# Kernel optimization log

Measured on AMD Instinct MI355X. Metric: run time of the kernel, lower is better.

## Reference

```python
import jax, jax.numpy as jnp
import numpy as np

B, L, D, DF, E, R = 4, 1024, 1024, 4096, 32768, 64
EPS = 1e-6


def layer_norm(x, g, b, eps=EPS):
    mu = x.mean(-1, keepdims=True)
    var = ((x - mu) ** 2).mean(-1, keepdims=True)
    return (x - mu) * jax.lax.rsqrt(var + eps) * g + b


def setup_inputs() -> dict:
    key = jax.random.key(0)
    ks = jax.random.split(key, 16)
    s = 0.02
    return {
        "hidden_states": jax.random.normal(ks[0], (B, L, D), jnp.float32),
        "rel_table": jax.random.normal(ks[1], (R, D), jnp.float32) * s,
        "Wq": jax.random.normal(ks[2], (D, D), jnp.float32) * s,
        "bq": jnp.zeros((D,), jnp.float32),
        "Wk": jax.random.normal(ks[3], (D, D), jnp.float32) * s,
        "Wv": jax.random.normal(ks[4], (D, D), jnp.float32) * s,
        "Wo": jax.random.normal(ks[5], (D, D), jnp.float32) * s,
        "bo": jnp.zeros((D,), jnp.float32),
        "ln0_g": jnp.ones((D,), jnp.float32),
        "ln0_b": jnp.zeros((D,), jnp.float32),
        "ln1_g": jnp.ones((D,), jnp.float32),
        "ln1_b": jnp.zeros((D,), jnp.float32),
        "W1": jax.random.normal(ks[6], (D, DF), jnp.float32) * s,
        "b1": jnp.zeros((DF,), jnp.float32),
        "W2": jax.random.normal(ks[7], (DF, D), jnp.float32) * s,
        "b2": jnp.zeros((D,), jnp.float32),
        "ln2_g": jnp.ones((D,), jnp.float32),
        "ln2_b": jnp.zeros((D,), jnp.float32),
        "edge_src": jax.random.randint(ks[8], (B, E), 0, L, jnp.int32),
        "edge_dst": jax.random.randint(ks[9], (B, E), 0, L, jnp.int32),
        "edge_rel": jax.random.randint(ks[10], (B, E), 0, R, jnp.int32),
    }


def reference(hidden_states, rel_table, Wq, bq, Wk, Wv, Wo, bo,
              ln0_g, ln0_b, ln1_g, ln1_b, W1, b1, W2, b2, ln2_g, ln2_b,
              edge_src, edge_dst, edge_rel):
    scale = np.sqrt(D).astype(np.float32)  # num_heads=1 -> d_k = D
    hs_norm = layer_norm(hidden_states, ln0_g, ln0_b)

    def rgat_one(x, src, dst, rel):
        # x: [L, D]; src/dst/rel: [E]
        e = rel_table[rel]                       # [E, D] relation embeddings
        q = x @ Wq + bq
        k = x @ Wk
        v = x @ Wv
        score = jnp.sum((k[src] + e) * q[dst], axis=-1) / scale      # [E]
        score = jnp.exp(jnp.clip(score, -10.0, 10.0))
        wv = jax.ops.segment_sum((v[src] + e) * score[:, None], dst, num_segments=L)
        z = jax.ops.segment_sum(score, dst, num_segments=L)          # [L]
        o = wv / z[:, None]
        out = layer_norm(x + o @ Wo + bo, ln1_g, ln1_b)
        ffn = jnp.maximum(out @ W1 + b1, 0.0) @ W2 + b2
        return layer_norm(out + ffn, ln2_g, ln2_b)

    graph_rep = jax.vmap(rgat_one)(hs_norm, edge_src, edge_dst, edge_rel)
    out = jax.nn.elu(graph_rep)                  # dropout = identity (eval)
    return hidden_states + out
```

## Files before the change

kernel.cpp:

```cpp
#include <hip/hip_runtime.h>
#include <hip/hip_bf16.h>

#define B_SZ 4
#define L_SEQ 1024
#define D_MODEL 1024
#define DF_FF 4096
#define E_PER_B 32768
#define R_REL 64
#define M_ROWS (B_SZ * L_SEQ)

typedef __attribute__((ext_vector_type(8))) short bf16x8;
typedef __attribute__((ext_vector_type(4))) float f32x4;

__device__ inline float b2f(unsigned short u) {
    union { unsigned int i; float f; } x; x.i = ((unsigned int)u) << 16; return x.f;
}
__device__ inline unsigned short f2b(float f) {
    union { float f; unsigned int u; } x; x.f = f;
    unsigned int r = x.u + 0x7FFFu + ((x.u >> 16) & 1u);
    return (unsigned short)(r >> 16);
}

#define GLOBAL_CAST(p) ((const __attribute__((address_space(1))) void*)(p))
#define LDS_CAST(p)    ((__attribute__((address_space(3))) void*)(p))

#define BT_QKV (1024u * 3072u)
#define SEXT_M 1152
#define LDA_WV 1088
#define LDB_WVP 1152
#define BT_WVP (1024u * 1152u)

__global__ void prep_all(const float* __restrict__ Wq, const float* __restrict__ Wk,
                         const float* __restrict__ Wv, const float* __restrict__ Wo,
                         const float* __restrict__ W1, const float* __restrict__ W2,
                         const float* __restrict__ rel, const float* __restrict__ bq,
                         const float* __restrict__ hidden,
                         const float* __restrict__ ln0_g, const float* __restrict__ ln0_b,
                         unsigned short* __restrict__ Wqkv_t, unsigned short* __restrict__ Wo_t,
                         unsigned short* __restrict__ W1_t, unsigned short* __restrict__ W2_t,
                         unsigned short* __restrict__ relbPad,
                         float* __restrict__ bqkv,
                         unsigned short* __restrict__ Xn_b16,
                         float* __restrict__ zeroReg) {
    __shared__ float tile[32][33];
    __shared__ float sb1[4], sb2[4];
    const int id = blockIdx.x, tid = threadIdx.x;
    if (id < 12288) {
        const float* src; unsigned short* dst; int K, N, x, y;
        if (id < 4096) {
            const int seg = id >> 10, t = id & 1023;
            K = 1024; N = 1024; x = t & 31; y = t >> 5;
            src = (seg == 0) ? Wq : (seg == 1) ? Wk : (seg == 2) ? Wv : Wo;
            dst = (seg == 3) ? Wo_t : (Wqkv_t + (size_t)seg * 1048576);
        } else if (id < 8192) {
            const int t = id - 4096; K = 1024; N = 4096; x = t & 127; y = t >> 7;
            src = W1; dst = W1_t;
        } else {
            const int t = id - 8192; K = 4096; N = 1024; x = t & 31; y = t >> 5;
            src = W2; dst = W2_t;
        }
        const int n0 = x * 32, k0 = y * 32, tx = tid & 31, ty = tid >> 5;
#pragma unroll
        for (int r = 0; r < 32; r += 8)
            tile[ty + r][tx] = src[(size_t)(k0 + ty + r) * N + (n0 + tx)];
        __syncthreads();
#pragma unroll
        for (int r = 0; r < 32; r += 8)
            dst[(size_t)(n0 + ty + r) * K + (k0 + tx)] = f2b(tile[tx][ty + r]);
    } else if (id < 12800) {
        const int i = (id - 12288) * 256 + tid;
        relbPad[i] = (i < 65536) ? f2b(rel[i]) : (unsigned short)0;
    } else if (id < 12812) {
        const int i = (id - 12800) * 256 + tid;
        bqkv[i] = (i < 1024) ? bq[i] : 0.0f;
    } else if (id < 16908) {
        const int row = id - 12812, t = tid;
        const size_t base = (size_t)row * 1024 + t * 4;
        float4 xv = *(const float4*)(hidden + base);
        float x0 = xv.x, x1 = xv.y, x2 = xv.z, x3 = xv.w;
        float s = x0 + x1 + x2 + x3;
#pragma unroll
        for (int o = 32; o > 0; o >>= 1) s += __shfl_down(s, o);
        if ((t & 63) == 0) sb1[t >> 6] = s;
        __syncthreads();
        const float mu = (sb1[0] + sb1[1] + sb1[2] + sb1[3]) * (1.0f / 1024.0f);
        const float d0 = x0 - mu, d1 = x1 - mu, d2 = x2 - mu, d3 = x3 - mu;
        float s2 = d0 * d0 + d1 * d1 + d2 * d2 + d3 * d3;
#pragma unroll
        for (int o = 32; o > 0; o >>= 1) s2 += __shfl_down(s2, o);
        if ((t & 63) == 0) sb2[t >> 6] = s2;
        __syncthreads();
        const float var = (sb2[0] + sb2[1] + sb2[2] + sb2[3]) * (1.0f / 1024.0f);
        const float rstd = rsqrtf(var + 1e-6f);
        const float4 gv = *(const float4*)(ln0_g + t * 4);
        const float4 bv = *(const float4*)(ln0_b + t * 4);
        ushort4 ob;
        ob.x = f2b(d0 * rstd * gv.x + bv.x);
        ob.y = f2b(d1 * rstd * gv.y + bv.y);
        ob.z = f2b(d2 * rstd * gv.z + bv.z);
        ob.w = f2b(d3 * rstd * gv.w + bv.w);
        *(ushort4*)(Xn_b16 + base) = ob;
    } else {
        const size_t base = (size_t)(id - 16908) * 4096 + tid * 4;
        const float4 z4 = make_float4(0.f, 0.f, 0.f, 0.f);
#pragma unroll
        for (int j = 0; j < 4; j++)
            *(float4*)(zeroReg + base + j * 1024) = z4;
    }
}

__device__ inline void tile_swizzle(int id, int ntn, int& tm, int& tn) {
    tm = ((id & 7) + ((id >> 3) / ntn) * 8) * 128;
    tn = ((id >> 3) % ntn) * 128;
}
__device__ inline void tsw256(int id, int ntn, int& tm, int& tn) {
    tm = ((id & 7) + ((id >> 3) / ntn) * 8) * 256;
    tn = ((id >> 3) % ntn) * 256;
}

#define GEMM_BODY(GA, LDA_, GB, LDB_, KLEN)                                                 \
    f32x4 acc[4][4];                                                                        \
    _Pragma("unroll") for (int i = 0; i < 4; i++)                                           \
        _Pragma("unroll") for (int j = 0; j < 4; j++) acc[i][j] = (f32x4)0.0f;              \
    for (int k0 = 0; k0 < (KLEN); k0 += 64) {                                               \
        __syncthreads();                                                                    \
        _Pragma("unroll") for (int r = 0; r < 4; ++r) {                                     \
            __builtin_amdgcn_global_load_lds(GLOBAL_CAST((GA) + (size_t)r * 8 * (LDA_)),    \
                LDS_CAST(&lA[(wave * 32 + r * 8) * 64]), 16, 0, 0);                         \
            __builtin_amdgcn_global_load_lds(GLOBAL_CAST((GB) + (size_t)r * 8 * (LDB_)),    \
                LDS_CAST(&lB[(wave * 32 + r * 8) * 64]), 16, 0, 0);                         \
        }                                                                                   \
        (GA) += 64; (GB) += 64;                                                             \
        __builtin_amdgcn_s_waitcnt(0);                                                      \
        __syncthreads();                                                                    \
        _Pragma("unroll") for (int kk = 0; kk < 2; ++kk) {                                  \
            const int cb = kk * 4 + quad;                                                   \
            bf16x8 af[4], bf[4];                                                            \
            _Pragma("unroll") for (int i = 0; i < 4; i++) {                                 \
                const int ra = wm + i * 16 + l16;                                           \
                af[i] = *(const bf16x8*)&lA[ra * 64 + ((cb ^ (ra & 7)) * 8)];               \
                const int rb = wn + i * 16 + l16;                                           \
                bf[i] = *(const bf16x8*)&lB[rb * 64 + ((cb ^ (rb & 7)) * 8)];               \
            }                                                                               \
            _Pragma("unroll") for (int mi = 0; mi < 4; mi++)                                \
                _Pragma("unroll") for (int ni = 0; ni < 4; ni++)                            \
                    acc[mi][ni] = __builtin_amdgcn_mfma_f32_16x16x32_bf16(                  \
                        af[mi], bf[ni], acc[mi][ni], 0, 0, 0);                              \
        }                                                                                   \
    }

#define ST_Aq(bufc, QM, kt) { \
    _Pragma("unroll") for (int j_ = 0; j_ < 2; j_++) { \
        const int u_ = j_ * 8 + wv; \
        const int lr_ = ((u_ >> 3) * 128) + (QM) * 64 + ((u_ & 7) * 8); \
        __builtin_amdgcn_global_load_lds(GLOBAL_CAST(Ag + (size_t)lr_ * lda + (kt) * 64), \
            LDS_CAST(&ls[bufc][0][lr_ * 64]), 16, 0, 0); } }
#define ST_Bq(bufc, QN, kt) { \
    _Pragma("unroll") for (int j_ = 0; j_ < 2; j_++) { \
        const int u_ = j_ * 8 + wv; \
        const int lr_ = ((u_ >> 2) * 64) + (QN) * 32 + ((u_ & 3) * 8); \
        __builtin_amdgcn_global_load_lds(GLOBAL_CAST(Bg + (size_t)lr_ * ldb + (kt) * 64), \
            LDS_CAST(&ls[bufc][1][lr_ * 64]), 16, 0, 0); } }

#define RD_Af(bufc, QM) { \
    _Pragma("unroll") for (int m4_ = 0; m4_ < 4; m4_++) \
        _Pragma("unroll") for (int kk_ = 0; kk_ < 2; kk_++) \
            af[m4_][kk_] = *(const bf16x8*)&ls[bufc][0][ \
                (wm * 128 + (QM) * 64 + m4_ * 16 + l16) * 64 + (((kk_ * 4 + quad) ^ (l16 & 7)) * 8)]; }
#define RD_Bs(SLOT, bufc, QN) { \
    _Pragma("unroll") for (int n2_ = 0; n2_ < 2; n2_++) \
        _Pragma("unroll") for (int kk_ = 0; kk_ < 2; kk_++) \
            SLOT[n2_][kk_] = *(const bf16x8*)&ls[bufc][1][ \
                (wc * 64 + (QN) * 32 + n2_ * 16 + l16) * 64 + (((kk_ * 4 + quad) ^ (l16 & 7)) * 8)]; }

#define VM2 asm volatile("s_waitcnt vmcnt(2)" ::: "memory");
#define VM0 asm volatile("s_waitcnt vmcnt(0)" ::: "memory");
#define LG8 asm volatile("s_waitcnt lgkmcnt(8)" ::: "memory");

#define MMCL(QM, QN, BS) \
    __builtin_amdgcn_s_setprio(1); \
    _Pragma("unroll") for (int m4_ = 0; m4_ < 4; m4_++) \
        _Pragma("unroll") for (int n2_ = 0; n2_ < 2; n2_++) \
            _Pragma("unroll") for (int kk_ = 0; kk_ < 2; kk_++) \
                acc[(QM) * 4 + m4_][(QN) * 2 + n2_] = __builtin_amdgcn_mfma_f32_16x16x32_bf16( \
                    af[m4_][kk_], BS[n2_][kk_], acc[(QM) * 4 + m4_][(QN) * 2 + n2_], 0, 0, 0); \
    __builtin_amdgcn_s_setprio(0);

#define PH2(STMT, READS, LGPRE, QM, QN, BS, VMW) { \
    STMT; \
    READS; \
    LGPRE; \
    __builtin_amdgcn_s_barrier(); \
    asm volatile("s_waitcnt lgkmcnt(0)" ::: "memory"); \
    __builtin_amdgcn_sched_barrier(0); \
    MMCL(QM, QN, BS) \
    VMW; \
    __builtin_amdgcn_s_barrier(); }

template<bool RELU, bool SPLITK>
__global__ __launch_bounds__(512, 2)
void gemm256(const unsigned short* __restrict__ A, int lda,
             const unsigned short* __restrict__ Bt, int ldb,
             const float* __restrict__ bias,
             unsigned short* __restrict__ C, size_t pstride,
             int N, int Kc, int ntn) {
    __shared__ unsigned short ls[2][2][16384];
    int tile_m, tile_n;
    tsw256(blockIdx.x, ntn, tile_m, tile_n);
    const int t = threadIdx.x;
    const int wv = t >> 6, lane = t & 63;
    const int wm = wv >> 2;
    const int wc = wv & 3;
    const int quad = lane >> 4, l16 = lane & 15;
    const int srow8 = lane >> 3;
    const int schunk = ((lane & 7) ^ srow8) * 8;
    const int z = SPLITK ? blockIdx.z : 0;
    const int kofs = z * Kc;

    const unsigned short* Ag = A + (size_t)(tile_m + srow8) * lda + kofs + schunk;
    const unsigned short* Bg = Bt + (size_t)(tile_n + srow8) * ldb + kofs + schunk;

    f32x4 acc[8][4];
#pragma unroll
    for (int i = 0; i < 8; i++)
#pragma unroll
        for (int j = 0; j < 4; j++) acc[i][j] = (f32x4)0.0f;
    bf16x8 af[4][2], b0f[2][2], b1f[2][2];

    ST_Aq(0, 0, 0) ST_Bq(0, 0, 0) ST_Bq(0, 1, 0) ST_Aq(0, 1, 0)
    VM0
    __builtin_amdgcn_s_barrier();

    const int NT = Kc >> 6;
    for (int tt = 0; tt < NT - 1; ++tt) {
        const int c = tt & 1, nb = c ^ 1;
        PH2(ST_Aq(nb, 0, tt + 1), RD_Af(c, 0) RD_Bs(b0f, c, 0), LG8, 0, 0, b0f, VM2)
        PH2(ST_Bq(nb, 0, tt + 1), RD_Bs(b1f, c, 1),            ,    0, 1, b1f, VM2)
        PH2(ST_Bq(nb, 1, tt + 1), RD_Af(c, 1),                 ,    1, 1, b1f, VM2)
        PH2(ST_Aq(nb, 1, tt + 1), ,                            ,    1, 0, b0f, VM2)
    }
    {
        const int c = (NT - 1) & 1;
        PH2(, RD_Af(c, 0) RD_Bs(b0f, c, 0), LG8, 0, 0, b0f, VM0)
        PH2(, RD_Bs(b1f, c, 1),            ,    0, 1, b1f, )
        PH2(, RD_Af(c, 1),                 ,    1, 1, b1f, )
        PH2(, ,                            ,    1, 0, b0f, )
    }

    unsigned short* Co = C + (SPLITK ? (size_t)z * pstride : 0);
#pragma unroll
    for (int mi = 0; mi < 8; mi++) {
#pragma unroll
        for (int ni = 0; ni < 4; ni++) {
            const int col = tile_n + wc * 64 + ni * 16 + l16;
            const float bv = (SPLITK && z != 0) ? 0.0f : bias[col];
#pragma unroll
            for (int r = 0; r < 4; r++) {
                const int row = tile_m + wm * 128 + mi * 16 + quad * 4 + r;
                float v = acc[mi][ni][r] + bv;
                if (RELU) v = fmaxf(v, 0.0f);
                Co[(size_t)row * N + col] = f2b(v);
            }
        }
    }
}

__global__ __launch_bounds__(256, 4)
void sext_w(const unsigned short* __restrict__ QKV,
            const unsigned short* __restrict__ relPad,
            const unsigned short* __restrict__ Wo_t,
            unsigned short* __restrict__ Pbase,
            unsigned short* __restrict__ Bwvp, int Kc) {
    __shared__ unsigned short lA[128 * 64];
    __shared__ unsigned short lB[128 * 64];
    const int id = blockIdx.x, t = threadIdx.x;
    const int wave = t >> 6, lane = t & 63;
    const int wm = (wave >> 1) * 64, wn = (wave & 1) * 64;
    const int quad = lane >> 4, l16 = lane & 15;
    const int srow = lane >> 3;
    const int schunk = ((lane & 7) ^ srow) * 8;

    if (id >= 576) {
        const int t2 = id - 576;
        const int b = t2 / 72, rem = t2 % 72;
        const int tile_m = (rem / 9) * 128;
        const int tile_n = (rem % 9) * 128;
        const unsigned short* gA = Wo_t + (size_t)(tile_m + wave * 32 + srow) * 1024 + schunk;
        const int brow = tile_n + wave * 32 + srow;
        const unsigned short* gB;
        size_t ldb;
        if (tile_n < 1024) {
            gB = QKV + (size_t)b * BT_QKV + (size_t)brow * 3072 + 2048 + schunk;
            ldb = 3072;
        } else {
            gB = relPad + (size_t)(brow - 1024) * 1024 + schunk;
            ldb = 1024;
        }
        GEMM_BODY(gA, 1024, gB, ldb, 1024)
        unsigned short* P = Bwvp + (size_t)b * BT_WVP;
#pragma unroll
        for (int mi = 0; mi < 4; mi++) {
#pragma unroll
            for (int ni = 0; ni < 4; ni++) {
                const int col = tile_n + wn + ni * 16 + l16;
#pragma unroll
                for (int r = 0; r < 4; r++) {
                    const int row = tile_m + wm + mi * 16 + quad * 4 + r;
                    P[(size_t)row * LDB_WVP + col] = f2b(acc[mi][ni][r]);
                }
            }
        }
        return;
    }

    const int bx = id % 72, b = (id / 72) & 3, z = id / 288;
    const int tile_m = (bx >> 3) * 128;
    const int tile_n = (bx & 7) * 128;
    const int kofs = z * Kc;
    const int arow = tile_m + wave * 32 + srow;
    const unsigned short* gA;
    size_t lda;
    if (tile_m < 1024) {
        gA = QKV + (size_t)b * BT_QKV + (size_t)arow * 3072 + 1024 + kofs + schunk;
        lda = 3072;
    } else {
        gA = relPad + (size_t)(arow - 1024) * 1024 + kofs + schunk;
        lda = 1024;
    }
    const unsigned short* gB = QKV + (size_t)b * BT_QKV
                                   + (size_t)(tile_n + wave * 32 + srow) * 3072 + kofs + schunk;
    GEMM_BODY(gA, lda, gB, 3072, Kc)
    unsigned short* P = Pbase + ((size_t)z * B_SZ + b) * (SEXT_M * 1024);
#pragma unroll
    for (int mi = 0; mi < 4; mi++) {
#pragma unroll
        for (int ni = 0; ni < 4; ni++) {
            const int col = tile_n + wn + ni * 16 + l16;
#pragma unroll
            for (int r = 0; r < 4; r++) {
                const int row = tile_m + wm + mi * 16 + quad * 4 + r;
                P[(size_t)row * 1024 + col] = f2b(acc[mi][ni][r]);
            }
        }
    }
}

__global__ __launch_bounds__(256, 4)
void gemm_wv_splitk(const unsigned short* __restrict__ A,
                    const unsigned short* __restrict__ Bt,
                    const float* __restrict__ bias,
                    unsigned short* __restrict__ Pbase, size_t pstride) {
    __shared__ unsigned short lA[128 * 64];
    __shared__ unsigned short lB[128 * 64];
    int tile_m, tile_n;
    tile_swizzle(blockIdx.x, 8, tile_m, tile_n);
    const int z = blockIdx.z;
    const int kofs = z * 576;
    const int Kc = z ? 512 : 576;
    const int t = threadIdx.x;
    const int wave = t >> 6, lane = t & 63;
    const int wm = (wave >> 1) * 64, wn = (wave & 1) * 64;
    const int quad = lane >> 4, l16 = lane & 15;
    const int srow = lane >> 3;
    const int schunk = ((lane & 7) ^ srow) * 8;
    const unsigned short* gA = A + (size_t)(tile_m + wave * 32 + srow) * LDA_WV + kofs + schunk;
    const unsigned short* gB = Bt + (size_t)(tile_m >> 10) * BT_WVP
                                  + (size_t)(tile_n + wave * 32 + srow) * LDB_WVP + kofs + schunk;
    GEMM_BODY(gA, LDA_WV, gB, LDB_WVP, Kc)
    unsigned short* P = Pbase + (size_t)z * pstride;
#pragma unroll
    for (int mi = 0; mi < 4; mi++) {
#pragma unroll
        for (int ni = 0; ni < 4; ni++) {
            const int col = tile_n + wn + ni * 16 + l16;
            const float bv = (z == 0) ? bias[col] : 0.0f;
#pragma unroll
            for (int r = 0; r < 4; r++) {
                const int row = tile_m + wm + mi * 16 + quad * 4 + r;
                P[(size_t)row * 1024 + col] = f2b(acc[mi][ni][r] + bv);
            }
        }
    }
}

template<bool FINAL, int NR>
__global__ void ln_kernel(const unsigned short* __restrict__ Xb,
                          const unsigned short* __restrict__ Rbase, size_t rstride,
                          const float* __restrict__ g, const float* __restrict__ be,
                          unsigned short* __restrict__ ob16,
                          const float* __restrict__ hidden, float* __restrict__ fout) {
    __shared__ float sb1[4], sb2[4];
    const int row = blockIdx.x, t = threadIdx.x;
    const size_t base = (size_t)row * 1024 + t * 4;

    ushort4 xv = *(const ushort4*)(Xb + base);
    float x0 = b2f(xv.x), x1 = b2f(xv.y), x2 = b2f(xv.z), x3 = b2f(xv.w);
#pragma unroll
    for (int r = 0; r < NR; r++) {
        ushort4 rv = *(const ushort4*)(Rbase + r * rstride + base);
        x0 += b2f(rv.x); x1 += b2f(rv.y); x2 += b2f(rv.z); x3 += b2f(rv.w);
    }
    float s = x0 + x1 + x2 + x3;
#pragma unroll
    for (int o = 32; o > 0; o >>= 1) s += __shfl_down(s, o);
    if ((t & 63) == 0) sb1[t >> 6] = s;
    __syncthreads();
    const float mu = (sb1[0] + sb1[1] + sb1[2] + sb1[3]) * (1.0f / 1024.0f);

    const float d0 = x0 - mu, d1 = x1 - mu, d2 = x2 - mu, d3 = x3 - mu;
    float s2 = d0 * d0 + d1 * d1 + d2 * d2 + d3 * d3;
#pragma unroll
    for (int o = 32; o > 0; o >>= 1) s2 += __shfl_down(s2, o);
    if ((t & 63) == 0) sb2[t >> 6] = s2;
    __syncthreads();
    const float var = (sb2[0] + sb2[1] + sb2[2] + sb2[3]) * (1.0f / 1024.0f);
    const float rstd = rsqrtf(var + 1e-6f);

    const float4 gv = *(const float4*)(g + t * 4);
    const float4 bv = *(const float4*)(be + t * 4);
    const float y0 = d0 * rstd * gv.x + bv.x;
    const float y1 = d1 * rstd * gv.y + bv.y;
    const float y2 = d2 * rstd * gv.z + bv.z;
    const float y3 = d3 * rstd * gv.w + bv.w;

    if (!FINAL) {
        ushort4 ob; ob.x = f2b(y0); ob.y = f2b(y1); ob.z = f2b(y2); ob.w = f2b(y3);
        *(ushort4*)(ob16 + base) = ob;
    } else {
        const float4 hv = *(const float4*)(hidden + base);
        const float e0 = y0 > 0.0f ? y0 : expm1f(y0);
        const float e1 = y1 > 0.0f ? y1 : expm1f(y1);
        const float e2 = y2 > 0.0f ? y2 : expm1f(y2);
        const float e3 = y3 > 0.0f ? y3 : expm1f(y3);
        float4 o; o.x = hv.x + e0; o.y = hv.y + e1; o.z = hv.z + e2; o.w = hv.w + e3;
        *(float4*)(fout + base) = o;
    }
}

__global__ void edge_scatter(const unsigned short* __restrict__ S,
                             const int* __restrict__ src, const int* __restrict__ dst,
                             const int* __restrict__ rel,
                             float* __restrict__ A, float* __restrict__ G) {
    const size_t ZSTR = (size_t)B_SZ * SEXT_M * 1024;
    const int gg = blockIdx.x * 256 + threadIdx.x;
    const int b = gg >> 15;
    const int s = src[gg], d = dst[gg], r = rel[gg];
    const size_t sbase = ((size_t)b * SEXT_M + s) * 1024 + d;
    const size_t tbase = ((size_t)b * SEXT_M + 1024 + r) * 1024 + d;
    const float sval = b2f(S[sbase]) + b2f(S[sbase + ZSTR]);
    const float tval = b2f(S[tbase]) + b2f(S[tbase + ZSTR]);
    float sc = (sval + tval) * (1.0f / 32.0f);
    sc = expf(fminf(fmaxf(sc, -10.0f), 10.0f));
    atomicAdd(&A[((size_t)((b << 10) + d) << 10) + s], sc);
    atomicAdd(&G[((size_t)((b << 10) + d) << 6) + r], sc);
}

__global__ void normalize(const float* __restrict__ A, const float* __restrict__ G,
                          unsigned short* __restrict__ Awv) {
    __shared__ float sInv;
    const int row = blockIdx.x, t = threadIdx.x;
    float v = 0.0f;
    if (t < 64) {
        v = G[(size_t)row * 64 + t];
        float s = v;
#pragma unroll
        for (int o = 1; o < 64; o <<= 1) s += __shfl_xor(s, o);
        if (t == 0) sInv = 1.0f / s;
    }
    __syncthreads();
    const float inv = sInv;
    const size_t obase = (size_t)row * LDA_WV;
    const float4 a = *(const float4*)(A + (size_t)row * 1024 + t * 4);
    ushort4 o;
    o.x = f2b(a.x * inv); o.y = f2b(a.y * inv); o.z = f2b(a.z * inv); o.w = f2b(a.w * inv);
    *(ushort4*)(Awv + obase + t * 4) = o;
    if (t < 16) {
        const float4 gq = *(const float4*)(G + (size_t)row * 64 + t * 4);
        ushort4 og;
        og.x = f2b(gq.x * inv); og.y = f2b(gq.y * inv);
        og.z = f2b(gq.z * inv); og.w = f2b(gq.w * inv);
        *(ushort4*)(Awv + obase + 1024 + t * 4) = og;
    }
}

extern "C" void kernel_launch(void* const* d_in, const int* in_sizes, int n_in,
                              void* d_out, int out_size, void* d_ws, size_t ws_size,
                              hipStream_t stream) {
    const float* hidden  = (const float*)d_in[0];
    const float* rel_tbl = (const float*)d_in[1];
    const float* Wq = (const float*)d_in[2];
    const float* bq = (const float*)d_in[3];
    const float* Wk = (const float*)d_in[4];
    const float* Wv = (const float*)d_in[5];
    const float* Wo = (const float*)d_in[6];
    const float* bo = (const float*)d_in[7];
    const float* ln0_g = (const float*)d_in[8];
    const float* ln0_b = (const float*)d_in[9];
    const float* ln1_g = (const float*)d_in[10];
    const float* ln1_b = (const float*)d_in[11];
    const float* W1 = (const float*)d_in[12];
    const float* b1 = (const float*)d_in[13];
    const float* W2 = (const float*)d_in[14];
    const float* b2 = (const float*)d_in[15];
    const float* ln2_g = (const float*)d_in[16];
    const float* ln2_b = (const float*)d_in[17];
    const int* esrc = (const int*)d_in[18];
    const int* edst = (const int*)d_in[19];
    const int* erel = (const int*)d_in[20];
    float* out = (float*)d_out;

    char* ws = (char*)d_ws;
    const size_t MB = 1024 * 1024;
    unsigned short* Xn_b16  = (unsigned short*)(ws + 16 * MB);
    unsigned short* H1      = (unsigned short*)(ws + 0);
    unsigned short* Wqkv_t  = (unsigned short*)(ws + 24 * MB);
    unsigned short* Wo_t    = (unsigned short*)(ws + 30 * MB);
    unsigned short* W1_t    = (unsigned short*)(ws + 32 * MB);
    unsigned short* W2_t    = (unsigned short*)(ws + 40 * MB);
    unsigned short* relbPad = (unsigned short*)(ws + 48 * MB);
    float*          bqkv    = (float*)(ws + 48 * MB + 512 * 1024);
    unsigned short* QKV     = (unsigned short*)(ws + 49 * MB);
    unsigned short* Awv     = (unsigned short*)(ws + 49 * MB);
    unsigned short* Qw2H    = (unsigned short*)(ws + 49 * MB);
    unsigned short* PwoH    = (unsigned short*)(ws + 66 * MB);
    unsigned short* SxH     = (unsigned short*)(ws + 73 * MB);
    unsigned short* Bwvp    = (unsigned short*)(ws + 92 * MB);
    float*          Amat    = (float*)(ws + 101 * MB);
    float*          Gmat    = (float*)(ws + 117 * MB);
    unsigned short* Out_b16 = (unsigned short*)(ws + 113 * MB);

    const size_t PSTRIDE_H = 4u * 1024 * 1024;
    const dim3 blk(256);
    const dim3 blk512(512);

    prep_all<<<17996, blk, 0, stream>>>(Wq, Wk, Wv, Wo, W1, W2, rel_tbl, bq,
                                        hidden, ln0_g, ln0_b,
                                        Wqkv_t, Wo_t, W1_t, W2_t, relbPad, bqkv,
                                        Xn_b16, Amat);
    gemm256<false, false><<<dim3(192), blk512, 0, stream>>>(
        Xn_b16, 1024, Wqkv_t, 1024, bqkv, QKV, 0, 3072, 1024, 12);
    sext_w<<<864, blk, 0, stream>>>(QKV, relbPad, Wo_t, SxH, Bwvp, 512);
    edge_scatter<<<512, blk, 0, stream>>>(SxH, esrc, edst, erel, Amat, Gmat);
    normalize<<<M_ROWS, blk, 0, stream>>>(Amat, Gmat, Awv);
    gemm_wv_splitk<<<dim3(256, 1, 2), blk, 0, stream>>>(Awv, Bwvp, bo, PwoH, PSTRIDE_H);
    ln_kernel<false, 2><<<M_ROWS, blk, 0, stream>>>(Xn_b16, PwoH, PSTRIDE_H, ln1_g, ln1_b,
                                                    Out_b16, nullptr, nullptr);
    gemm256<true, false><<<dim3(256), blk512, 0, stream>>>(
        Out_b16, 1024, W1_t, 1024, b1, H1, 0, 4096, 1024, 16);
    gemm256<false, true><<<dim3(64, 1, 4), blk512, 0, stream>>>(
        H1, 4096, W2_t, 4096, b2, Qw2H, PSTRIDE_H, 1024, 1024, 4);
    ln_kernel<true, 4><<<M_ROWS, blk, 0, stream>>>(Out_b16, Qw2H, PSTRIDE_H, ln2_g, ln2_b,
                                                   nullptr, hidden, out);
    (void)in_sizes; (void)n_in; (void)out_size; (void)ws_size;
}
```

Baseline: 349.9 us.

## Remove split-K from score GEMM and issue gemm256 loads earlier

The sext_w score GEMM no longer uses a two-way split-K. Each block now covers the full K=1024, so there are fewer blocks, no second partial buffer to write, and edge_scatter reads one bf16 value instead of adding two partials. Separately, the gemm256 main loop issues both A and B next-tile loads in the first two phases rather than one per phase, with adjusted vmcnt waits, to give memory loads more time in flight. The risks are lower parallelism in sext_w (576 blocks) and possible vmcnt ordering mistakes in the reshuffled pipeline.

```diff
diff --git a/kernel.cpp b/kernel.cpp
--- a/kernel.cpp
+++ b/kernel.cpp
@@ -173,8 +173,11 @@
             SLOT[n2_][kk_] = *(const bf16x8*)&ls[bufc][1][ \
                 (wc * 64 + (QN) * 32 + n2_ * 16 + l16) * 64 + (((kk_ * 4 + quad) ^ (l16 & 7)) * 8)]; }
 
+#define VM0 asm volatile("s_waitcnt vmcnt(0)" ::: "memory");
 #define VM2 asm volatile("s_waitcnt vmcnt(2)" ::: "memory");
-#define VM0 asm volatile("s_waitcnt vmcnt(0)" ::: "memory");
+#define VM4 asm volatile("s_waitcnt vmcnt(4)" ::: "memory");
+#define VM6 asm volatile("s_waitcnt vmcnt(6)" ::: "memory");
+#define VM8 asm volatile("s_waitcnt vmcnt(8)" ::: "memory");
 #define LG8 asm volatile("s_waitcnt lgkmcnt(8)" ::: "memory");
 
 #define MMCL(QM, QN, BS) \
@@ -234,15 +237,17 @@
     const int NT = Kc >> 6;
     for (int tt = 0; tt < NT - 1; ++tt) {
         const int c = tt & 1, nb = c ^ 1;
-        PH2(ST_Aq(nb, 0, tt + 1), RD_Af(c, 0) RD_Bs(b0f, c, 0), LG8, 0, 0, b0f, VM2)
-        PH2(ST_Bq(nb, 0, tt + 1), RD_Bs(b1f, c, 1),            ,    0, 1, b1f, VM2)
-        PH2(ST_Bq(nb, 1, tt + 1), RD_Af(c, 1),                 ,    1, 1, b1f, VM2)
-        PH2(ST_Aq(nb, 1, tt + 1), ,                            ,    1, 0, b0f, VM2)
+        PH2(ST_Aq(nb, 0, tt + 1) ST_Bq(nb, 0, tt + 1),
+            RD_Af(c, 0) RD_Bs(b0f, c, 0), LG8, 0, 0, b0f, VM6)
+        PH2(ST_Bq(nb, 1, tt + 1) ST_Aq(nb, 1, tt + 1),
+            RD_Bs(b1f, c, 1),            ,    0, 1, b1f, VM8)
+        PH2(, RD_Af(c, 1),               ,    1, 1, b1f, )
+        PH2(, ,                          ,    1, 0, b0f, VM4)
     }
     {
         const int c = (NT - 1) & 1;
-        PH2(, RD_Af(c, 0) RD_Bs(b0f, c, 0), LG8, 0, 0, b0f, VM0)
-        PH2(, RD_Bs(b1f, c, 1),            ,    0, 1, b1f, )
+        PH2(, RD_Af(c, 0) RD_Bs(b0f, c, 0), LG8, 0, 0, b0f, VM2)
+        PH2(, RD_Bs(b1f, c, 1),            ,    0, 1, b1f, VM0)
         PH2(, RD_Af(c, 1),                 ,    1, 1, b1f, )
         PH2(, ,                            ,    1, 0, b0f, )
     }
@@ -270,7 +275,7 @@
             const unsigned short* __restrict__ relPad,
             const unsigned short* __restrict__ Wo_t,
             unsigned short* __restrict__ Pbase,
-            unsigned short* __restrict__ Bwvp, int Kc) {
+            unsigned short* __restrict__ Bwvp) {
     __shared__ unsigned short lA[128 * 64];
     __shared__ unsigned short lB[128 * 64];
     const int id = blockIdx.x, t = threadIdx.x;
@@ -280,8 +285,8 @@
     const int srow = lane >> 3;
     const int schunk = ((lane & 7) ^ srow) * 8;
 
-    if (id >= 576) {
-        const int t2 = id - 576;
+    if (id >= 288) {
+        const int t2 = id - 288;
         const int b = t2 / 72, rem = t2 % 72;
         const int tile_m = (rem / 9) * 128;
         const int tile_n = (rem % 9) * 128;
@@ -313,24 +318,23 @@
         return;
     }
 
-    const int bx = id % 72, b = (id / 72) & 3, z = id / 288;
+    const int bx = id % 72, b = id / 72;
     const int tile_m = (bx >> 3) * 128;
     const int tile_n = (bx & 7) * 128;
-    const int kofs = z * Kc;
     const int arow = tile_m + wave * 32 + srow;
     const unsigned short* gA;
     size_t lda;
     if (tile_m < 1024) {
-        gA = QKV + (size_t)b * BT_QKV + (size_t)arow * 3072 + 1024 + kofs + schunk;
+        gA = QKV + (size_t)b * BT_QKV + (size_t)arow * 3072 + 1024 + schunk;
         lda = 3072;
     } else {
-        gA = relPad + (size_t)(arow - 1024) * 1024 + kofs + schunk;
+        gA = relPad + (size_t)(arow - 1024) * 1024 + schunk;
         lda = 1024;
     }
     const unsigned short* gB = QKV + (size_t)b * BT_QKV
-                                   + (size_t)(tile_n + wave * 32 + srow) * 3072 + kofs + schunk;
-    GEMM_BODY(gA, lda, gB, 3072, Kc)
-    unsigned short* P = Pbase + ((size_t)z * B_SZ + b) * (SEXT_M * 1024);
+                                   + (size_t)(tile_n + wave * 32 + srow) * 3072 + schunk;
+    GEMM_BODY(gA, lda, gB, 3072, 1024)
+    unsigned short* P = Pbase + (size_t)b * (SEXT_M * 1024);
 #pragma unroll
     for (int mi = 0; mi < 4; mi++) {
 #pragma unroll
@@ -441,14 +445,13 @@
                              const int* __restrict__ src, const int* __restrict__ dst,
                              const int* __restrict__ rel,
                              float* __restrict__ A, float* __restrict__ G) {
-    const size_t ZSTR = (size_t)B_SZ * SEXT_M * 1024;
     const int gg = blockIdx.x * 256 + threadIdx.x;
     const int b = gg >> 15;
     const int s = src[gg], d = dst[gg], r = rel[gg];
     const size_t sbase = ((size_t)b * SEXT_M + s) * 1024 + d;
     const size_t tbase = ((size_t)b * SEXT_M + 1024 + r) * 1024 + d;
-    const float sval = b2f(S[sbase]) + b2f(S[sbase + ZSTR]);
-    const float tval = b2f(S[tbase]) + b2f(S[tbase + ZSTR]);
+    const float sval = b2f(S[sbase]);
+    const float tval = b2f(S[tbase]);
     float sc = (sval + tval) * (1.0f / 32.0f);
     sc = expf(fminf(fmaxf(sc, -10.0f), 10.0f));
     atomicAdd(&A[((size_t)((b << 10) + d) << 10) + s], sc);
@@ -539,7 +542,7 @@
                                         Xn_b16, Amat);
     gemm256<false, false><<<dim3(192), blk512, 0, stream>>>(
         Xn_b16, 1024, Wqkv_t, 1024, bqkv, QKV, 0, 3072, 1024, 12);
-    sext_w<<<864, blk, 0, stream>>>(QKV, relbPad, Wo_t, SxH, Bwvp, 512);
+    sext_w<<<576, blk, 0, stream>>>(QKV, relbPad, Wo_t, SxH, Bwvp);
     edge_scatter<<<512, blk, 0, stream>>>(SxH, esrc, edst, erel, Amat, Gmat);
     normalize<<<M_ROWS, blk, 0, stream>>>(Amat, Gmat, Awv);
     gemm_wv_splitk<<<dim3(256, 1, 2), blk, 0, stream>>>(Awv, Bwvp, bo, PwoH, PSTRIDE_H);
```

Result: no change. 352.7 us (+0.8%).
